# Performance work log

Hardware: AMD Instinct MI355X
Metric: run time of the kernel (lower is better)

Reference implementation:

```python
import jax, jax.numpy as jnp
import numpy as np

N, E, DIN, DOUT = 40000, 640000, 128, 10


def _gat_layer(h_in, src, dst, W, a_src, a_dst, b, n_nodes):
    # h: [N, D]; edges include self-loops already
    h = h_in @ W
    alpha = jax.nn.leaky_relu((h @ a_src)[src] + (h @ a_dst)[dst], 0.2)  # [E']
    m = jax.ops.segment_max(alpha, dst, num_segments=n_nodes)
    e = jnp.exp(alpha - m[dst])
    s = jax.ops.segment_sum(e, dst, num_segments=n_nodes)
    coef = e / (s[dst] + 1e-16)
    out = jax.ops.segment_sum(h[src] * coef[:, None], dst, num_segments=n_nodes)
    return out + b


def setup_inputs() -> dict:
    key = jax.random.key(0)
    ks = jax.random.split(key, 20)
    p = lambda k, shp: (jax.random.normal(k, shp, dtype=jnp.float32) * 0.05)
    inp = {
        "x": jax.random.normal(ks[0], (N, DIN), dtype=jnp.float32),
        "edge_index": jax.random.randint(ks[1], (2, E), 0, N, dtype=jnp.int32),
        "batch": jnp.sort(jax.random.randint(ks[2], (N,), 0, 64, dtype=jnp.int32)),
        "edge_attr": jax.random.normal(ks[3], (E, 4), dtype=jnp.float32),
        # GATConv 1: 128 -> 64
        "W1": p(ks[4], (DIN, 64)), "a1s": p(ks[5], (64,)), "a1d": p(ks[6], (64,)), "b1": jnp.zeros((64,), jnp.float32),
        # GATConv 2: 64 -> 128
        "W2": p(ks[7], (64, 128)), "a2s": p(ks[8], (128,)), "a2d": p(ks[9], (128,)), "b2": jnp.zeros((128,), jnp.float32),
        # GATConv 3: 128 -> 128
        "W3": p(ks[10], (128, 128)), "a3s": p(ks[11], (128,)), "a3d": p(ks[12], (128,)), "b3": jnp.zeros((128,), jnp.float32),
        # SAGPooling scorer: GraphConv(128, 1)
        "wp_rel": p(ks[13], (128, 1)), "wp_root": p(ks[14], (128, 1)), "bp": jnp.zeros((1,), jnp.float32),
        # final Linear(128, out_channels)
        "Wl": p(ks[15], (128, DOUT)), "bl": jnp.zeros((DOUT,), jnp.float32),
    }
    return inp


def reference(x, edge_index, batch, edge_attr,
              W1, a1s, a1d, b1, W2, a2s, a2d, b2, W3, a3s, a3d, b3,
              wp_rel, wp_root, bp, Wl, bl):
    n = x.shape[0]
    src, dst = edge_index[0], edge_index[1]
    # GATConv adds self-loops (edge_attr unused: edge_dim=None)
    loops = jnp.arange(n, dtype=src.dtype)
    src_sl = jnp.concatenate([src, loops])
    dst_sl = jnp.concatenate([dst, loops])

    h = jax.nn.relu(_gat_layer(x, src_sl, dst_sl, W1, a1s, a1d, b1, n))
    h = jax.nn.relu(_gat_layer(h, src_sl, dst_sl, W2, a2s, a2d, b2, n))
    h = jax.nn.relu(_gat_layer(h, src_sl, dst_sl, W3, a3s, a3d, b3, n))

    # SAGPooling(ratio=1): score via GraphConv (no self-loops), tanh gating, all nodes kept
    agg = jax.ops.segment_sum(h[src], dst, num_segments=n)  # [N, 128]
    score = (agg @ wp_rel + h @ wp_root + bp)[:, 0]         # [N]
    h = h * jnp.tanh(score)[:, None]

    # dropout is identity in eval mode
    return jax.nn.relu(h @ Wl + bl)
```

## Files before the change

kernel.cpp:

```cpp
#include <hip/hip_runtime.h>
#include <math.h>

template<int K, int N, int NT>
__global__ __launch_bounds__(256) void gemm_tile(
    const float* __restrict__ A, const float* __restrict__ B,
    float* __restrict__ C, int M,
    const float* __restrict__ bias, const float* __restrict__ score, int outN,
    const float* __restrict__ va, const float* __restrict__ vb,
    float* __restrict__ outa, float* __restrict__ outb)
{
    static_assert(256 % NT == 0, "NT must divide 256");
    __shared__ float As[64 * K];
    const int tid = threadIdx.x;
    const int base = blockIdx.x * 64;
    for (int idx = tid; idx < 64 * K; idx += 256) {
        int r = idx / K, k = idx - r * K;
        int gr = base + r;
        As[idx] = (gr < M) ? A[(size_t)gr * K + k] : 0.f;
    }
    __syncthreads();
    constexpr int RSTEP = 256 / NT;
    constexpr int NR = 64 / RSTEP;
    const int c = tid % NT;
    const int r0 = tid / NT;
    const int col = blockIdx.y * NT + c;
    float acc[NR];
#pragma unroll
    for (int i = 0; i < NR; ++i) acc[i] = 0.f;
    const float4* As4 = reinterpret_cast<const float4*>(As);
    const float* Bc = B + col;
    float b0 = Bc[0 * N], b1 = Bc[1 * N], b2 = Bc[2 * N], b3 = Bc[3 * N];
    for (int k = 0; k < K; k += 4) {
        const int kn = (k + 4 < K) ? (k + 4) : k;
        float n0 = Bc[(kn + 0) * N];
        float n1 = Bc[(kn + 1) * N];
        float n2 = Bc[(kn + 2) * N];
        float n3 = Bc[(kn + 3) * N];
#pragma unroll
        for (int i = 0; i < NR; ++i) {
            float4 a = As4[((r0 + i * RSTEP) * K + k) >> 2];
            acc[i] = fmaf(a.x, b0, acc[i]);
            acc[i] = fmaf(a.y, b1, acc[i]);
            acc[i] = fmaf(a.z, b2, acc[i]);
            acc[i] = fmaf(a.w, b3, acc[i]);
        }
        b0 = n0; b1 = n1; b2 = n2; b3 = n3;
    }
    if (score == nullptr) {
#pragma unroll
        for (int i = 0; i < NR; ++i) {
            int gr = base + r0 + i * RSTEP;
            if (gr < M) C[(size_t)gr * N + col] = acc[i];
        }
    } else {
        if (col < outN) {
#pragma unroll
            for (int i = 0; i < NR; ++i) {
                int gr = base + r0 + i * RSTEP;
                if (gr < M) {
                    float v = tanhf(score[gr]) * acc[i] + bias[col];
                    C[(size_t)gr * outN + col] = fmaxf(v, 0.f);
                }
            }
        }
    }
    if (va != nullptr && blockIdx.y == 0) {
        const int w = tid >> 6;
        const int lane = tid & 63;
        for (int rr = 0; rr < 16; ++rr) {
            int r = w * 16 + rr;
            int gr = base + r;
            if (gr < M) {
                float sa = 0.f, sb = 0.f;
#pragma unroll
                for (int k = lane; k < K; k += 64) {
                    float av = As[r * K + k];
                    sa = fmaf(av, va[k], sa);
                    sb = fmaf(av, vb[k], sb);
                }
#pragma unroll
                for (int off = 32; off; off >>= 1) {
                    sa += __shfl_xor(sa, off);
                    sb += __shfl_xor(sb, off);
                }
                if (lane == 0) { outa[gr] = sa; outb[gr] = sb; }
            }
        }
    }
}

__global__ __launch_bounds__(256) void hist_deg(
    const int* __restrict__ dst, int* __restrict__ deg, int E, int n)
{
    int e = blockIdx.x * 256 + threadIdx.x;
    if (e >= E + n) return;
    int d = (e < E) ? dst[e] : (e - E);
    atomicAdd(deg + d, 1);
}

__global__ __launch_bounds__(256) void scan_local(
    const int* __restrict__ deg, int* __restrict__ row_start, int* __restrict__ blocksum, int n)
{
    __shared__ int s[256];
    const int t = threadIdx.x;
    const int i = blockIdx.x * 256 + t;
    int v = (i < n) ? deg[i] : 0;
    s[t] = v;
    __syncthreads();
#pragma unroll
    for (int off = 1; off < 256; off <<= 1) {
        int u = (t >= off) ? s[t - off] : 0;
        __syncthreads();
        s[t] += u;
        __syncthreads();
    }
    if (i < n) row_start[i] = s[t] - v;
    if (t == 255) blocksum[blockIdx.x] = s[255];
}

__global__ __launch_bounds__(256) void scan_blocks(int* __restrict__ blocksum, int nb)
{
    __shared__ int s[256];
    const int t = threadIdx.x;
    int v = (t < nb) ? blocksum[t] : 0;
    s[t] = v;
    __syncthreads();
#pragma unroll
    for (int off = 1; off < 256; off <<= 1) {
        int u = (t >= off) ? s[t - off] : 0;
        __syncthreads();
        s[t] += u;
        __syncthreads();
    }
    if (t < nb) blocksum[t] = s[t] - v;
}

__global__ __launch_bounds__(256) void scan_add(
    int* __restrict__ row_start, int* __restrict__ cursor,
    const int* __restrict__ blocksum, int n, int total)
{
    const int i = blockIdx.x * 256 + threadIdx.x;
    if (i < n) {
        int v = row_start[i] + blocksum[blockIdx.x];
        row_start[i] = v;
        cursor[i] = v;
    } else if (i == n) {
        row_start[n] = total;
    }
}

__global__ __launch_bounds__(256) void fill_csr(
    const int* __restrict__ src, const int* __restrict__ dst,
    int* __restrict__ cursor, int* __restrict__ csr_src, int E, int n)
{
    int e = blockIdx.x * 256 + threadIdx.x;
    if (e >= E + n) return;
    int s, d;
    if (e < E) { s = src[e]; d = dst[e]; } else { s = d = e - E; }
    int pos = atomicAdd(cursor + d, 1);
    csr_src[pos] = s;
}

template<int D, bool POOL>
__global__ __launch_bounds__(256) void gat_aggregate(
    const int* __restrict__ row_start, const int* __restrict__ csr_src,
    const float* __restrict__ asv, const float* __restrict__ adv,
    const float* __restrict__ h, const float* __restrict__ bias,
    float* __restrict__ out,
    const float* __restrict__ wpr, const float* __restrict__ wpo,
    float* __restrict__ poolA, float* __restrict__ poolB, int n)
{
    __shared__ float lds_e[4][128];
    __shared__ int   lds_i[4][128];
    const int node = (blockIdx.x * 256 + threadIdx.x) >> 6;
    const int lane = threadIdx.x & 63;
    const int w = threadIdx.x >> 6;
    if (node >= n) return;
    const int beg = row_start[node];
    const int deg = row_start[node + 1] - beg;
    const float advv = adv[node];
    const bool fast = (deg <= 128);

    float amax = -INFINITY;
    if (fast) {
        for (int j = lane; j < deg; j += 64) {
            int s = csr_src[beg + j];
            lds_i[w][j] = s;
            float a = asv[s] + advv;
            a = (a >= 0.f) ? a : 0.2f * a;
            lds_e[w][j] = a;
            amax = fmaxf(amax, a);
        }
    } else {
        for (int j = lane; j < deg; j += 64) {
            float a = asv[csr_src[beg + j]] + advv;
            a = (a >= 0.f) ? a : 0.2f * a;
            amax = fmaxf(amax, a);
        }
    }
#pragma unroll
    for (int off = 32; off; off >>= 1) amax = fmaxf(amax, __shfl_xor(amax, off));

    float ssum = 0.f;
    if (fast) {
        for (int j = lane; j < deg; j += 64) {
            float ev = expf(lds_e[w][j] - amax);
            lds_e[w][j] = ev;
            ssum += ev;
        }
    } else {
        for (int j = lane; j < deg; j += 64) {
            float a = asv[csr_src[beg + j]] + advv;
            a = (a >= 0.f) ? a : 0.2f * a;
            ssum += expf(a - amax);
        }
    }
#pragma unroll
    for (int off = 32; off; off >>= 1) ssum += __shfl_xor(ssum, off);
    const float inv = 1.f / (ssum + 1e-16f);

    if constexpr (D == 128) {
        const float2* h2 = reinterpret_cast<const float2*>(h);
        float2 a0 = {0.f, 0.f}, a1 = {0.f, 0.f}, a2 = {0.f, 0.f}, a3 = {0.f, 0.f};
        int j = 0;
        if (fast) {
            for (; j + 4 <= deg; j += 4) {
                int s0 = lds_i[w][j], s1 = lds_i[w][j + 1], s2 = lds_i[w][j + 2], s3 = lds_i[w][j + 3];
                float c0 = lds_e[w][j] * inv, c1 = lds_e[w][j + 1] * inv;
                float c2 = lds_e[w][j + 2] * inv, c3 = lds_e[w][j + 3] * inv;
                float2 v0 = h2[(size_t)s0 * 64 + lane];
                float2 v1 = h2[(size_t)s1 * 64 + lane];
                float2 v2 = h2[(size_t)s2 * 64 + lane];
                float2 v3 = h2[(size_t)s3 * 64 + lane];
                a0.x = fmaf(v0.x, c0, a0.x); a0.y = fmaf(v0.y, c0, a0.y);
                a1.x = fmaf(v1.x, c1, a1.x); a1.y = fmaf(v1.y, c1, a1.y);
                a2.x = fmaf(v2.x, c2, a2.x); a2.y = fmaf(v2.y, c2, a2.y);
                a3.x = fmaf(v3.x, c3, a3.x); a3.y = fmaf(v3.y, c3, a3.y);
            }
            for (; j < deg; ++j) {
                int s = lds_i[w][j];
                float c = lds_e[w][j] * inv;
                float2 v = h2[(size_t)s * 64 + lane];
                a0.x = fmaf(v.x, c, a0.x); a0.y = fmaf(v.y, c, a0.y);
            }
        } else {
            for (; j < deg; ++j) {
                int s = csr_src[beg + j];
                float a = asv[s] + advv;
                a = (a >= 0.f) ? a : 0.2f * a;
                float c = expf(a - amax) * inv;
                float2 v = h2[(size_t)s * 64 + lane];
                a0.x = fmaf(v.x, c, a0.x); a0.y = fmaf(v.y, c, a0.y);
            }
        }
        float2 o;
        o.x = fmaxf(((a0.x + a1.x) + (a2.x + a3.x)) + bias[2 * lane], 0.f);
        o.y = fmaxf(((a0.y + a1.y) + (a2.y + a3.y)) + bias[2 * lane + 1], 0.f);
        reinterpret_cast<float2*>(out)[(size_t)node * 64 + lane] = o;
        if constexpr (POOL) {
            float pa = fmaf(o.x, wpr[2 * lane], o.y * wpr[2 * lane + 1]);
            float pb = fmaf(o.x, wpo[2 * lane], o.y * wpo[2 * lane + 1]);
#pragma unroll
            for (int off = 32; off; off >>= 1) {
                pa += __shfl_xor(pa, off);
                pb += __shfl_xor(pb, off);
            }
            if (lane == 0) { poolA[node] = pa; poolB[node] = pb; }
        }
    } else {
        float a0 = 0.f, a1 = 0.f, a2 = 0.f, a3 = 0.f;
        int j = 0;
        if (fast) {
            for (; j + 4 <= deg; j += 4) {
                int s0 = lds_i[w][j], s1 = lds_i[w][j + 1], s2 = lds_i[w][j + 2], s3 = lds_i[w][j + 3];
                float c0 = lds_e[w][j] * inv, c1 = lds_e[w][j + 1] * inv;
                float c2 = lds_e[w][j + 2] * inv, c3 = lds_e[w][j + 3] * inv;
                a0 = fmaf(h[(size_t)s0 * D + lane], c0, a0);
                a1 = fmaf(h[(size_t)s1 * D + lane], c1, a1);
                a2 = fmaf(h[(size_t)s2 * D + lane], c2, a2);
                a3 = fmaf(h[(size_t)s3 * D + lane], c3, a3);
            }
            for (; j < deg; ++j) {
                a0 = fmaf(h[(size_t)lds_i[w][j] * D + lane], lds_e[w][j] * inv, a0);
            }
        } else {
            for (; j < deg; ++j) {
                int s = csr_src[beg + j];
                float a = asv[s] + advv;
                a = (a >= 0.f) ? a : 0.2f * a;
                float c = expf(a - amax) * inv;
                a0 = fmaf(h[(size_t)s * D + lane], c, a0);
            }
        }
        out[(size_t)node * D + lane] = fmaxf(((a0 + a1) + (a2 + a3)) + bias[lane], 0.f);
    }
}

__global__ __launch_bounds__(256) void score_csr(
    const int* __restrict__ row_start, const int* __restrict__ csr_src,
    const float* __restrict__ ts, const float* __restrict__ td,
    const float* __restrict__ bp, float* __restrict__ score, int n)
{
    int i = blockIdx.x * 256 + threadIdx.x;
    if (i >= n) return;
    int beg = row_start[i], end = row_start[i + 1];
    float s = td[i] + bp[0] - ts[i];
    for (int j = beg; j < end; ++j) s += ts[csr_src[j]];
    score[i] = s;
}

__global__ __launch_bounds__(256) void precompute(
    const float* __restrict__ W1, const float* __restrict__ a1s, const float* __restrict__ a1d,
    const float* __restrict__ W2, const float* __restrict__ a2s, const float* __restrict__ a2d,
    const float* __restrict__ W3, const float* __restrict__ a3s, const float* __restrict__ a3d,
    const float* __restrict__ Wl, const float* __restrict__ bl,
    float* __restrict__ va1, float* __restrict__ vb1,
    float* __restrict__ va2, float* __restrict__ vb2,
    float* __restrict__ va3, float* __restrict__ vb3,
    float* __restrict__ Wlp, float* __restrict__ blp,
    int* __restrict__ deg, int n)
{
    int t = blockIdx.x * 256 + threadIdx.x;
    if (t < n) deg[t] = 0;
    if (t < 128) {
        float sa = 0.f, sb = 0.f;
        for (int j = 0; j < 64; ++j) {
            float w = W1[t * 64 + j];
            sa = fmaf(w, a1s[j], sa); sb = fmaf(w, a1d[j], sb);
        }
        va1[t] = sa; vb1[t] = sb;
    } else if (t < 192) {
        int k = t - 128;
        float sa = 0.f, sb = 0.f;
        for (int j = 0; j < 128; ++j) {
            float w = W2[k * 128 + j];
            sa = fmaf(w, a2s[j], sa); sb = fmaf(w, a2d[j], sb);
        }
        va2[k] = sa; vb2[k] = sb;
    } else if (t < 320) {
        int k = t - 192;
        float sa = 0.f, sb = 0.f;
        for (int j = 0; j < 128; ++j) {
            float w = W3[k * 128 + j];
            sa = fmaf(w, a3s[j], sa); sb = fmaf(w, a3d[j], sb);
        }
        va3[k] = sa; vb3[k] = sb;
    } else if (t < 320 + 2048) {
        int i = t - 320;
        int k = i >> 4, c = i & 15;
        Wlp[i] = (c < 10) ? Wl[k * 10 + c] : 0.f;
    } else if (t < 320 + 2048 + 16) {
        int c = t - (320 + 2048);
        blp[c] = (c < 10) ? bl[c] : 0.f;
    }
}

extern "C" void kernel_launch(void* const* d_in, const int* in_sizes, int n_in,
                              void* d_out, int out_size, void* d_ws, size_t ws_size,
                              hipStream_t stream) {
    const float* x   = (const float*)d_in[0];
    const int*   ei  = (const int*)d_in[1];
    const float* W1  = (const float*)d_in[4];
    const float* a1s = (const float*)d_in[5];
    const float* a1d = (const float*)d_in[6];
    const float* b1  = (const float*)d_in[7];
    const float* W2  = (const float*)d_in[8];
    const float* a2s = (const float*)d_in[9];
    const float* a2d = (const float*)d_in[10];
    const float* b2  = (const float*)d_in[11];
    const float* W3  = (const float*)d_in[12];
    const float* a3s = (const float*)d_in[13];
    const float* a3d = (const float*)d_in[14];
    const float* b3  = (const float*)d_in[15];
    const float* wpr = (const float*)d_in[16];
    const float* wpo = (const float*)d_in[17];
    const float* bp  = (const float*)d_in[18];
    const float* Wl  = (const float*)d_in[19];
    const float* bl  = (const float*)d_in[20];

    const int n = in_sizes[0] / 128;
    const int E = in_sizes[1] / 2;
    const int Esl = E + n;
    const int* src = ei;
    const int* dst = ei + E;

    float* ws = (float*)d_ws;
    const size_t nd = (size_t)n * 128;
    float* bufA      = ws;
    float* bufB      = bufA + nd;
    float* asv       = bufB + nd;
    float* adv       = asv + n;
    float* tsv       = adv + n;
    float* tdv       = tsv + n;
    float* score     = tdv + n;
    int*   deg       = (int*)(score + n);
    int*   row_start = deg + n;
    int*   cursor    = row_start + n + 1;
    int*   blocksum  = cursor + n;
    int*   csr_src   = blocksum + 256;
    float* va1       = (float*)(csr_src + Esl);
    float* vb1       = va1 + 128;
    float* va2       = vb1 + 128;
    float* vb2       = va2 + 64;
    float* va3       = vb2 + 64;
    float* vb3       = va3 + 128;
    float* Wlp       = vb3 + 128;
    float* blp       = Wlp + 128 * 16;

    const unsigned EB = (unsigned)((Esl + 255) / 256);
    const unsigned NB = (unsigned)((n + 255) / 256);
    const unsigned MB = (unsigned)((n + 63) / 64);
    const unsigned WB = (unsigned)(((size_t)n * 64 + 255) / 256);

    precompute<<<NB, 256, 0, stream>>>(W1, a1s, a1d, W2, a2s, a2d, W3, a3s, a3d, Wl, bl,
                                       va1, vb1, va2, vb2, va3, vb3, Wlp, blp, deg, n);
    hist_deg<<<EB, 256, 0, stream>>>(dst, deg, E, n);
    scan_local<<<NB, 256, 0, stream>>>(deg, row_start, blocksum, n);
    scan_blocks<<<1, 256, 0, stream>>>(blocksum, (int)NB);
    scan_add<<<NB, 256, 0, stream>>>(row_start, cursor, blocksum, n, Esl);
    fill_csr<<<EB, 256, 0, stream>>>(src, dst, cursor, csr_src, E, n);

    gemm_tile<128, 64, 64><<<dim3(MB, 1), 256, 0, stream>>>(
        x, W1, bufA, n, nullptr, nullptr, 0, va1, vb1, asv, adv);
    gat_aggregate<64, false><<<WB, 256, 0, stream>>>(row_start, csr_src, asv, adv, bufA, b1, bufB,
                                                     nullptr, nullptr, nullptr, nullptr, n);

    gemm_tile<64, 128, 64><<<dim3(MB, 2), 256, 0, stream>>>(
        bufB, W2, bufA, n, nullptr, nullptr, 0, va2, vb2, asv, adv);
    gat_aggregate<128, false><<<WB, 256, 0, stream>>>(row_start, csr_src, asv, adv, bufA, b2, bufB,
                                                      nullptr, nullptr, nullptr, nullptr, n);

    gemm_tile<128, 128, 64><<<dim3(MB, 2), 256, 0, stream>>>(
        bufB, W3, bufA, n, nullptr, nullptr, 0, va3, vb3, asv, adv);
    gat_aggregate<128, true><<<WB, 256, 0, stream>>>(row_start, csr_src, asv, adv, bufA, b3, bufB,
                                                     wpr, wpo, tsv, tdv, n);

    score_csr<<<NB, 256, 0, stream>>>(row_start, csr_src, tsv, tdv, bp, score, n);
    gemm_tile<128, 16, 16><<<dim3(MB, 1), 256, 0, stream>>>(
        bufB, Wlp, (float*)d_out, n, blp, score, 10, nullptr, nullptr, nullptr, nullptr);
}
```

Before: 353.9 us.

## Replace GAT layer GEMMs with register-tiled kernel fusing attention projections

```diff
diff --git a/kernel.cpp b/kernel.cpp
--- a/kernel.cpp
+++ b/kernel.cpp
@@ -1,15 +1,147 @@
 #include <hip/hip_runtime.h>
 #include <math.h>
+
+template<int K, int N>
+__global__ __launch_bounds__(128) void gemm_rt(
+    const float* __restrict__ A, const float* __restrict__ B,
+    float* __restrict__ C, int M,
+    const float* __restrict__ va, const float* __restrict__ vb,
+    float* __restrict__ outa, float* __restrict__ outb)
+{
+    constexpr int KC = 32;
+    constexpr int NC = K / KC;
+    constexpr int TC = N / 8;
+    constexpr int TR = 128 / TC;
+    constexpr int MR = 64 / TR;
+    constexpr int KT = KC / TC;
+    constexpr int AST = 68;
+
+    __shared__ float AsT[KC * AST];
+    __shared__ float Bs[KC * N];
+
+    const int tid = threadIdx.x;
+    const int base = blockIdx.x * 64;
+    const int tc = tid % TC;
+    const int tr = tid / TC;
+    const int sq = tid & 7;
+    const int sr = tid >> 3;
+
+    float acc[MR][8];
+#pragma unroll
+    for (int m = 0; m < MR; ++m)
+#pragma unroll
+        for (int j = 0; j < 8; ++j) acc[m][j] = 0.f;
+    float sa[MR], sb[MR];
+#pragma unroll
+    for (int m = 0; m < MR; ++m) { sa[m] = 0.f; sb[m] = 0.f; }
+
+    for (int ch = 0; ch < NC; ++ch) {
+        const int k0 = ch * KC;
+#pragma unroll
+        for (int rr = sr; rr < 64; rr += 16) {
+            int gr = base + rr;
+            float4 av = (gr < M) ? *(const float4*)(A + (size_t)gr * K + k0 + 4 * sq)
+                                 : make_float4(0.f, 0.f, 0.f, 0.f);
+            AsT[(4 * sq + 0) * AST + rr] = av.x;
+            AsT[(4 * sq + 1) * AST + rr] = av.y;
+            AsT[(4 * sq + 2) * AST + rr] = av.z;
+            AsT[(4 * sq + 3) * AST + rr] = av.w;
+        }
+#pragma unroll
+        for (int t = tid; t < KC * N / 4; t += 128) {
+            int f = t * 4;
+            int k = f / N, c = f % N;
+            *(float4*)(Bs + k * N + c) = *(const float4*)(B + (size_t)(k0 + k) * N + c);
+        }
+        __syncthreads();
+
+#pragma unroll 4
+        for (int kk = 0; kk < KC; ++kk) {
+            const float* ap = AsT + kk * AST + MR * tr;
+            const float* bp = Bs + kk * N + 8 * tc;
+            float4 b0 = *(const float4*)(bp);
+            float4 b1 = *(const float4*)(bp + 4);
+            float4 a0 = *(const float4*)(ap);
+#pragma unroll
+            for (int m = 0; m < 4; ++m) {
+                float av = ((const float*)&a0)[m];
+                acc[m][0] = fmaf(av, b0.x, acc[m][0]);
+                acc[m][1] = fmaf(av, b0.y, acc[m][1]);
+                acc[m][2] = fmaf(av, b0.z, acc[m][2]);
+                acc[m][3] = fmaf(av, b0.w, acc[m][3]);
+                acc[m][4] = fmaf(av, b1.x, acc[m][4]);
+                acc[m][5] = fmaf(av, b1.y, acc[m][5]);
+                acc[m][6] = fmaf(av, b1.z, acc[m][6]);
+                acc[m][7] = fmaf(av, b1.w, acc[m][7]);
+            }
+            if constexpr (MR == 8) {
+                float4 a1 = *(const float4*)(ap + 4);
+#pragma unroll
+                for (int m = 0; m < 4; ++m) {
+                    float av = ((const float*)&a1)[m];
+                    acc[m + 4][0] = fmaf(av, b0.x, acc[m + 4][0]);
+                    acc[m + 4][1] = fmaf(av, b0.y, acc[m + 4][1]);
+                    acc[m + 4][2] = fmaf(av, b0.z, acc[m + 4][2]);
+                    acc[m + 4][3] = fmaf(av, b0.w, acc[m + 4][3]);
+                    acc[m + 4][4] = fmaf(av, b1.x, acc[m + 4][4]);
+                    acc[m + 4][5] = fmaf(av, b1.y, acc[m + 4][5]);
+                    acc[m + 4][6] = fmaf(av, b1.z, acc[m + 4][6]);
+                    acc[m + 4][7] = fmaf(av, b1.w, acc[m + 4][7]);
+                }
+            }
+        }
+        if (va != nullptr) {
+#pragma unroll
+            for (int kl = 0; kl < KT; ++kl) {
+                int k = tc * KT + kl;
+                float av_ = va[k0 + k];
+                float bv_ = vb[k0 + k];
+#pragma unroll
+                for (int m = 0; m < MR; ++m) {
+                    float aval = AsT[k * AST + MR * tr + m];
+                    sa[m] = fmaf(aval, av_, sa[m]);
+                    sb[m] = fmaf(aval, bv_, sb[m]);
+                }
+            }
+        }
+        __syncthreads();
+    }
+
+#pragma unroll
+    for (int m = 0; m < MR; ++m) {
+        int gr = base + MR * tr + m;
+        if (gr < M) {
+            float4 o0 = make_float4(acc[m][0], acc[m][1], acc[m][2], acc[m][3]);
+            float4 o1 = make_float4(acc[m][4], acc[m][5], acc[m][6], acc[m][7]);
+            *(float4*)(C + (size_t)gr * N + 8 * tc) = o0;
+            *(float4*)(C + (size_t)gr * N + 8 * tc + 4) = o1;
+        }
+    }
+    if (va != nullptr) {
+#pragma unroll
+        for (int m = 0; m < MR; ++m) {
+#pragma unroll
+            for (int off = TC / 2; off; off >>= 1) {
+                sa[m] += __shfl_xor(sa[m], off);
+                sb[m] += __shfl_xor(sb[m], off);
+            }
+        }
+        if (tc == 0) {
+#pragma unroll
+            for (int m = 0; m < MR; ++m) {
+                int gr = base + MR * tr + m;
+                if (gr < M) { outa[gr] = sa[m]; outb[gr] = sb[m]; }
+            }
+        }
+    }
+}
 
 template<int K, int N, int NT>
 __global__ __launch_bounds__(256) void gemm_tile(
     const float* __restrict__ A, const float* __restrict__ B,
     float* __restrict__ C, int M,
-    const float* __restrict__ bias, const float* __restrict__ score, int outN,
-    const float* __restrict__ va, const float* __restrict__ vb,
-    float* __restrict__ outa, float* __restrict__ outb)
-{
-    static_assert(256 % NT == 0, "NT must divide 256");
+    const float* __restrict__ bias, const float* __restrict__ score, int outN)
+{
     __shared__ float As[64 * K];
     const int tid = threadIdx.x;
     const int base = blockIdx.x * 64;
@@ -23,12 +155,11 @@
     constexpr int NR = 64 / RSTEP;
     const int c = tid % NT;
     const int r0 = tid / NT;
-    const int col = blockIdx.y * NT + c;
     float acc[NR];
 #pragma unroll
     for (int i = 0; i < NR; ++i) acc[i] = 0.f;
     const float4* As4 = reinterpret_cast<const float4*>(As);
-    const float* Bc = B + col;
+    const float* Bc = B + c;
     float b0 = Bc[0 * N], b1 = Bc[1 * N], b2 = Bc[2 * N], b3 = Bc[3 * N];
     for (int k = 0; k < K; k += 4) {
         const int kn = (k + 4 < K) ? (k + 4) : k;
@@ -46,44 +177,13 @@
         }
         b0 = n0; b1 = n1; b2 = n2; b3 = n3;
     }
-    if (score == nullptr) {
+    if (c < outN) {
 #pragma unroll
         for (int i = 0; i < NR; ++i) {
             int gr = base + r0 + i * RSTEP;
-            if (gr < M) C[(size_t)gr * N + col] = acc[i];
-        }
-    } else {
-        if (col < outN) {
-#pragma unroll
-            for (int i = 0; i < NR; ++i) {
-                int gr = base + r0 + i * RSTEP;
-                if (gr < M) {
-                    float v = tanhf(score[gr]) * acc[i] + bias[col];
-                    C[(size_t)gr * outN + col] = fmaxf(v, 0.f);
-                }
-            }
-        }
-    }
-    if (va != nullptr && blockIdx.y == 0) {
-        const int w = tid >> 6;
-        const int lane = tid & 63;
-        for (int rr = 0; rr < 16; ++rr) {
-            int r = w * 16 + rr;
-            int gr = base + r;
             if (gr < M) {
-                float sa = 0.f, sb = 0.f;
-#pragma unroll
-                for (int k = lane; k < K; k += 64) {
-                    float av = As[r * K + k];
-                    sa = fmaf(av, va[k], sa);
-                    sb = fmaf(av, vb[k], sb);
-                }
-#pragma unroll
-                for (int off = 32; off; off >>= 1) {
-                    sa += __shfl_xor(sa, off);
-                    sb += __shfl_xor(sb, off);
-                }
-                if (lane == 0) { outa[gr] = sa; outb[gr] = sb; }
+                float v = tanhf(score[gr]) * acc[i] + bias[c];
+                C[(size_t)gr * outN + c] = fmaxf(v, 0.f);
             }
         }
     }
@@ -420,22 +520,18 @@
     scan_add<<<NB, 256, 0, stream>>>(row_start, cursor, blocksum, n, Esl);
     fill_csr<<<EB, 256, 0, stream>>>(src, dst, cursor, csr_src, E, n);
 
-    gemm_tile<128, 64, 64><<<dim3(MB, 1), 256, 0, stream>>>(
-        x, W1, bufA, n, nullptr, nullptr, 0, va1, vb1, asv, adv);
+    gemm_rt<128, 64><<<MB, 128, 0, stream>>>(x, W1, bufA, n, va1, vb1, asv, adv);
     gat_aggregate<64, false><<<WB, 256, 0, stream>>>(row_start, csr_src, asv, adv, bufA, b1, bufB,
                                                      nullptr, nullptr, nullptr, nullptr, n);
 
-    gemm_tile<64, 128, 64><<<dim3(MB, 2), 256, 0, stream>>>(
-        bufB, W2, bufA, n, nullptr, nullptr, 0, va2, vb2, asv, adv);
+    gemm_rt<64, 128><<<MB, 128, 0, stream>>>(bufB, W2, bufA, n, va2, vb2, asv, adv);
     gat_aggregate<128, false><<<WB, 256, 0, stream>>>(row_start, csr_src, asv, adv, bufA, b2, bufB,
                                                       nullptr, nullptr, nullptr, nullptr, n);
 
-    gemm_tile<128, 128, 64><<<dim3(MB, 2), 256, 0, stream>>>(
-        bufB, W3, bufA, n, nullptr, nullptr, 0, va3, vb3, asv, adv);
+    gemm_rt<128, 128><<<MB, 128, 0, stream>>>(bufB, W3, bufA, n, va3, vb3, asv, adv);
     gat_aggregate<128, true><<<WB, 256, 0, stream>>>(row_start, csr_src, asv, adv, bufA, b3, bufB,
                                                      wpr, wpo, tsv, tdv, n);
 
     score_csr<<<NB, 256, 0, stream>>>(row_start, csr_src, tsv, tdv, bp, score, n);
-    gemm_tile<128, 16, 16><<<dim3(MB, 1), 256, 0, stream>>>(
-        bufB, Wlp, (float*)d_out, n, blp, score, 10, nullptr, nullptr, nullptr, nullptr);
-}
+    gemm_tile<128, 16, 16><<<MB, 256, 0, stream>>>(bufB, Wlp, (float*)d_out, n, blp, score, 10);
+}
```

New measurement: 333.6 us. -5.7%, faster.
